# Optimization experiments

Measured on AMD Instinct MI355X. Metric: run time of the kernel, lower is better.

Reference implementation:

```python
import jax, jax.numpy as jnp
import numpy as np

E = 8        # num_experts
D_IN = 512   # num_inputs
H = 256      # num_neurons_expert
T = 64       # num_neurons_tower
B = 16384    # batch


def setup_inputs() -> dict:
    key = jax.random.key(0)
    ks = jax.random.split(key, 7)
    s_in = 1.0 / np.sqrt(D_IN)
    s_h = 1.0 / np.sqrt(H)
    return {
        "xv": jax.random.normal(ks[0], (B, D_IN), dtype=jnp.float32),
        # expert weights stacked: torch Linear weight is (out,in) -> (E, H, D_IN)
        "We": jax.random.uniform(ks[1], (E, H, D_IN), jnp.float32, -s_in, s_in),
        "be": jax.random.uniform(ks[2], (E, H), jnp.float32, -s_in, s_in),
        "Wg": jax.random.uniform(ks[3], (E, D_IN), jnp.float32, -s_in, s_in),
        "bg": jax.random.uniform(ks[4], (E,), jnp.float32, -s_in, s_in),
        "Wt": jax.random.uniform(ks[5], (T, H), jnp.float32, -s_h, s_h),
        "bt": jax.random.uniform(ks[6], (T,), jnp.float32, -s_h, s_h),
    }


def reference(xv, We, be, Wg, bg, Wt, bt):
    # All experts as one batched GEMM: [B,D] x [E,H,D] -> [B,E,H]
    experts = jax.nn.relu(jnp.einsum("bd,ehd->beh", xv, We) + be[None, :, :])
    # Dropout is identity in eval mode.
    gate = jax.nn.softmax(xv @ Wg.T + bg, axis=1)            # [B,E]
    combined = jnp.einsum("beh,be->bh", experts, gate)        # [B,H]
    out = jax.nn.sigmoid(combined @ Wt.T + bt)                # [B,T]
    return out
```

## Files before the change

### kernel.cpp

```cpp
#include <hip/hip_runtime.h>
#include <hip/hip_bf16.h>
#include <stdint.h>

typedef unsigned short u16;
typedef __bf16 bf16x8 __attribute__((ext_vector_type(8)));
typedef float f32x4 __attribute__((ext_vector_type(4)));

#define LDS_A_USH 8192
#define LDS_B_USH 16384

__device__ __forceinline__ void glds16(const void* g, void* l) {
  __builtin_amdgcn_global_load_lds(
      (const __attribute__((address_space(1))) unsigned int*)g,
      (__attribute__((address_space(3))) unsigned int*)l, 16, 0, 0);
}

__device__ __forceinline__ u16 f2bf(float f) {
  unsigned int u = __builtin_bit_cast(unsigned int, f);
  u += 0x7fffu + ((u >> 16) & 1u);
  return (u16)(u >> 16);
}

__global__ __launch_bounds__(256) void prep_kernel(
    const float* __restrict__ xv, const float* __restrict__ We,
    const float* __restrict__ Wg, const float* __restrict__ bg,
    const float* __restrict__ Wt,
    u16* __restrict__ xv_bf, u16* __restrict__ We_bf,
    u16* __restrict__ Wt_bf, float* __restrict__ gate) {
  const int bx = blockIdx.x;
  if (bx < 4096) {
    const int wid = threadIdx.x >> 6, lane = threadIdx.x & 63;
    const int row = bx * 4 + wid;
    const float* xr = xv + (row << 9) + lane * 8;
    float4 x0 = *(const float4*)xr;
    float4 x1 = *(const float4*)(xr + 4);
    uint4 o;
    o.x = (unsigned)f2bf(x0.x) | ((unsigned)f2bf(x0.y) << 16);
    o.y = (unsigned)f2bf(x0.z) | ((unsigned)f2bf(x0.w) << 16);
    o.z = (unsigned)f2bf(x1.x) | ((unsigned)f2bf(x1.y) << 16);
    o.w = (unsigned)f2bf(x1.z) | ((unsigned)f2bf(x1.w) << 16);
    *(uint4*)(xv_bf + (row << 9) + lane * 8) = o;
    float s[8];
#pragma unroll
    for (int e = 0; e < 8; e++) {
      const float* wg = Wg + (e << 9) + lane * 8;
      float4 w0 = *(const float4*)wg;
      float4 w1 = *(const float4*)(wg + 4);
      s[e] = x0.x * w0.x + x0.y * w0.y + x0.z * w0.z + x0.w * w0.w +
             x1.x * w1.x + x1.y * w1.y + x1.z * w1.z + x1.w * w1.w;
    }
#pragma unroll
    for (int e = 0; e < 8; e++) {
#pragma unroll
      for (int off = 32; off > 0; off >>= 1) s[e] += __shfl_xor(s[e], off);
      s[e] += bg[e];
    }
    float mx = s[0];
#pragma unroll
    for (int e = 1; e < 8; e++) mx = fmaxf(mx, s[e]);
    float p[8], sum = 0.f;
#pragma unroll
    for (int e = 0; e < 8; e++) { p[e] = __expf(s[e] - mx); sum += p[e]; }
    float inv = 1.f / sum;
    if (lane == 0) {
      float4 g0 = {p[0] * inv, p[1] * inv, p[2] * inv, p[3] * inv};
      float4 g1 = {p[4] * inv, p[5] * inv, p[6] * inv, p[7] * inv};
      *(float4*)(gate + row * 8) = g0;
      *(float4*)(gate + row * 8 + 4) = g1;
    }
  } else {
    const int base = (bx - 4096) * 2048 + threadIdx.x * 8;
    const float* src;
    u16* dst;
    if (base < 1048576) { src = We + base; dst = We_bf + base; }
    else { src = Wt + (base - 1048576); dst = Wt_bf + (base - 1048576); }
    float4 a = *(const float4*)src;
    float4 b = *(const float4*)(src + 4);
    uint4 o;
    o.x = (unsigned)f2bf(a.x) | ((unsigned)f2bf(a.y) << 16);
    o.y = (unsigned)f2bf(a.z) | ((unsigned)f2bf(a.w) << 16);
    o.z = (unsigned)f2bf(b.x) | ((unsigned)f2bf(b.y) << 16);
    o.w = (unsigned)f2bf(b.z) | ((unsigned)f2bf(b.w) << 16);
    *(uint4*)dst = o;
  }
}

__global__ __launch_bounds__(256, 2) void moe_main(
    const u16* __restrict__ xv_bf, const u16* __restrict__ We_bf,
    const float* __restrict__ be, const float* __restrict__ gate,
    const u16* __restrict__ Wt_bf, float* __restrict__ part) {
  __shared__ u16 lds[LDS_A_USH + LDS_B_USH];

  const int bx = blockIdx.x;
  const int mb = bx >> 1;
  const int hb = bx & 1;
  const int m0 = mb << 6;
  const int tid = threadIdx.x;
  const int lane = tid & 63;
  const int wid = tid >> 6;
  const int wm = wid >> 1;
  const int wn = wid & 1;
  const int l15 = lane & 15;
  const int l4 = lane >> 4;

  f32x4 comb[2][4];
#pragma unroll
  for (int mt = 0; mt < 2; mt++)
#pragma unroll
    for (int nt = 0; nt < 4; nt++) comb[mt][nt] = {0.f, 0.f, 0.f, 0.f};

  for (int e = 0; e < 8; e++) {
    f32x4 acc[2][4];
#pragma unroll
    for (int mt = 0; mt < 2; mt++)
#pragma unroll
      for (int nt = 0; nt < 4; nt++) acc[mt][nt] = {0.f, 0.f, 0.f, 0.f};

    const u16* Wb = We_bf + (e << 17);
    for (int kc = 0; kc < 4; kc++) {
      __syncthreads();
      const int kofs = kc << 7;
#pragma unroll
      for (int r = 0; r < 4; r++) {
        int gi = r * 256 + tid;
        int m = gi >> 4, s = gi & 15;
        int g = (s & 8) | ((s & 7) ^ (m & 7));
        glds16(xv_bf + ((m0 + m) << 9) + kofs + (g << 3), &lds[gi << 3]);
      }
#pragma unroll
      for (int r = 0; r < 8; r++) {
        int gi = r * 256 + tid;
        int n = gi >> 4, s = gi & 15;
        int g = (s & 8) | ((s & 7) ^ (n & 7));
        glds16(Wb + (((hb << 7) + n) << 9) + kofs + (g << 3),
               &lds[LDS_A_USH + (gi << 3)]);
      }
      __syncthreads();
#pragma unroll
      for (int ks = 0; ks < 4; ks++) {
        const int gg = ks * 4 + l4;
        bf16x8 af[2], bfr[4];
#pragma unroll
        for (int mt = 0; mt < 2; mt++) {
          int row = wm * 32 + mt * 16 + l15;
          int slot = (gg & 8) | ((gg & 7) ^ (row & 7));
          af[mt] = *(const bf16x8*)&lds[(row << 7) + (slot << 3)];
        }
#pragma unroll
        for (int nt = 0; nt < 4; nt++) {
          int n = wn * 64 + nt * 16 + l15;
          int slot = (gg & 8) | ((gg & 7) ^ (n & 7));
          bfr[nt] = *(const bf16x8*)&lds[LDS_A_USH + (n << 7) + (slot << 3)];
        }
#pragma unroll
        for (int mt = 0; mt < 2; mt++)
#pragma unroll
          for (int nt = 0; nt < 4; nt++)
            acc[mt][nt] = __builtin_amdgcn_mfma_f32_16x16x32_bf16(
                af[mt], bfr[nt], acc[mt][nt], 0, 0, 0);
      }
    }
    float bev[4];
#pragma unroll
    for (int nt = 0; nt < 4; nt++)
      bev[nt] = be[(e << 8) + (hb << 7) + wn * 64 + nt * 16 + l15];
#pragma unroll
    for (int mt = 0; mt < 2; mt++) {
#pragma unroll
      for (int i = 0; i < 4; i++) {
        float g = gate[((m0 + wm * 32 + mt * 16 + l4 * 4 + i) << 3) + e];
#pragma unroll
        for (int nt = 0; nt < 4; nt++)
          comb[mt][nt][i] += g * fmaxf(acc[mt][nt][i] + bev[nt], 0.f);
      }
    }
  }

  __syncthreads();
#pragma unroll
  for (int mt = 0; mt < 2; mt++)
#pragma unroll
    for (int i = 0; i < 4; i++) {
      int row = wm * 32 + mt * 16 + l4 * 4 + i;
#pragma unroll
      for (int nt = 0; nt < 4; nt++) {
        int col = wn * 64 + nt * 16 + l15;
        __bf16 v = (__bf16)comb[mt][nt][i];
        lds[row * 136 + col] = __builtin_bit_cast(u16, v);
      }
    }
  __syncthreads();
  f32x4 tacc[4];
#pragma unroll
  for (int nt = 0; nt < 4; nt++) tacc[nt] = {0.f, 0.f, 0.f, 0.f};
  const u16* WtB = Wt_bf + (hb << 7);
#pragma unroll
  for (int kc = 0; kc < 4; kc++) {
    int ko = kc * 32 + l4 * 8;
    bf16x8 aT = *(const bf16x8*)&lds[(wid * 16 + l15) * 136 + ko];
#pragma unroll
    for (int nt = 0; nt < 4; nt++) {
      bf16x8 bT = *(const bf16x8*)&WtB[(nt * 16 + l15) * 256 + ko];
      tacc[nt] = __builtin_amdgcn_mfma_f32_16x16x32_bf16(aT, bT, tacc[nt], 0, 0, 0);
    }
  }
  float* pout = part + hb * 1048576;
#pragma unroll
  for (int nt = 0; nt < 4; nt++)
#pragma unroll
    for (int i = 0; i < 4; i++) {
      int grow = m0 + wid * 16 + l4 * 4 + i;
      pout[grow * 64 + nt * 16 + l15] = tacc[nt][i];
    }
}

__global__ __launch_bounds__(256) void finish_kernel(
    const float* __restrict__ part, const float* __restrict__ bt,
    float* __restrict__ out) {
  const int idx = (blockIdx.x * 256 + threadIdx.x) << 2;
  float4 a = *(const float4*)(part + idx);
  float4 b = *(const float4*)(part + 1048576 + idx);
  float4 c = *(const float4*)(bt + (idx & 63));
  float4 r;
  r.x = 1.f / (1.f + __expf(-(a.x + b.x + c.x)));
  r.y = 1.f / (1.f + __expf(-(a.y + b.y + c.y)));
  r.z = 1.f / (1.f + __expf(-(a.z + b.z + c.z)));
  r.w = 1.f / (1.f + __expf(-(a.w + b.w + c.w)));
  *(float4*)(out + idx) = r;
}

extern "C" void kernel_launch(void* const* d_in, const int* in_sizes, int n_in,
                              void* d_out, int out_size, void* d_ws, size_t ws_size,
                              hipStream_t stream) {
  const float* xv = (const float*)d_in[0];
  const float* We = (const float*)d_in[1];
  const float* be = (const float*)d_in[2];
  const float* Wg = (const float*)d_in[3];
  const float* bg = (const float*)d_in[4];
  const float* Wt = (const float*)d_in[5];
  const float* bt = (const float*)d_in[6];

  char* ws = (char*)d_ws;
  u16* xv_bf = (u16*)ws;
  u16* We_bf = (u16*)(ws + 16777216);
  u16* Wt_bf = (u16*)(ws + 18874368);
  float* gate = (float*)(ws + 18907136);
  float* part = (float*)(ws + 19431424);

  prep_kernel<<<4616, 256, 0, stream>>>(xv, We, Wg, bg, Wt, xv_bf, We_bf, Wt_bf, gate);
  moe_main<<<512, 256, 0, stream>>>(xv_bf, We_bf, be, gate, Wt_bf, part);
  finish_kernel<<<1024, 256, 0, stream>>>(part, bt, (float*)d_out);
}
```

Measured before the change: 152.4 us.

## Restructure MoE kernel: 128-row tiles, expert-group split, bf16 partials, separate gate kernel

The main kernel now uses 512-thread blocks on 128-row tiles. Each block covers one half of H and one group of 4 experts, holding per-expert accumulators so an A tile loaded into LDS is reused across 4 experts per K chunk. The gate softmax moves into its own kernel that reads the bf16 copy of xv. Partials are written as bf16 across 4 splits and summed in the finish kernel, which reduces partial-store traffic but adds bf16 rounding, an extra launch, and more register pressure from 32 accumulator tiles.

```diff
diff --git a/kernel.cpp b/kernel.cpp
--- a/kernel.cpp
+++ b/kernel.cpp
@@ -1,13 +1,13 @@
 #include <hip/hip_runtime.h>
-#include <hip/hip_bf16.h>
 #include <stdint.h>
 
 typedef unsigned short u16;
 typedef __bf16 bf16x8 __attribute__((ext_vector_type(8)));
 typedef float f32x4 __attribute__((ext_vector_type(4)));
 
-#define LDS_A_USH 8192
-#define LDS_B_USH 16384
+#define XV_N 8388608
+#define WE_N 1048576
+#define WT_N 16384
 
 __device__ __forceinline__ void glds16(const void* g, void* l) {
   __builtin_amdgcn_global_load_lds(
@@ -21,212 +21,262 @@
   return (u16)(u >> 16);
 }
 
-__global__ __launch_bounds__(256) void prep_kernel(
+__device__ __forceinline__ float bf2f(u16 u) {
+  return __builtin_bit_cast(float, ((unsigned int)u) << 16);
+}
+
+__global__ __launch_bounds__(256) void convert_kernel(
     const float* __restrict__ xv, const float* __restrict__ We,
-    const float* __restrict__ Wg, const float* __restrict__ bg,
-    const float* __restrict__ Wt,
-    u16* __restrict__ xv_bf, u16* __restrict__ We_bf,
-    u16* __restrict__ Wt_bf, float* __restrict__ gate) {
-  const int bx = blockIdx.x;
-  if (bx < 4096) {
-    const int wid = threadIdx.x >> 6, lane = threadIdx.x & 63;
-    const int row = bx * 4 + wid;
-    const float* xr = xv + (row << 9) + lane * 8;
-    float4 x0 = *(const float4*)xr;
-    float4 x1 = *(const float4*)(xr + 4);
-    uint4 o;
-    o.x = (unsigned)f2bf(x0.x) | ((unsigned)f2bf(x0.y) << 16);
-    o.y = (unsigned)f2bf(x0.z) | ((unsigned)f2bf(x0.w) << 16);
-    o.z = (unsigned)f2bf(x1.x) | ((unsigned)f2bf(x1.y) << 16);
-    o.w = (unsigned)f2bf(x1.z) | ((unsigned)f2bf(x1.w) << 16);
-    *(uint4*)(xv_bf + (row << 9) + lane * 8) = o;
-    float s[8];
+    const float* __restrict__ Wt, u16* __restrict__ dst) {
+  int idx = (blockIdx.x * 256 + threadIdx.x) * 8;
+  const float* src;
+  if (idx < XV_N) src = xv + idx;
+  else if (idx < XV_N + WE_N) src = We + (idx - XV_N);
+  else src = Wt + (idx - XV_N - WE_N);
+  float4 a = *(const float4*)src;
+  float4 b = *(const float4*)(src + 4);
+  uint4 o;
+  o.x = (unsigned)f2bf(a.x) | ((unsigned)f2bf(a.y) << 16);
+  o.y = (unsigned)f2bf(a.z) | ((unsigned)f2bf(a.w) << 16);
+  o.z = (unsigned)f2bf(b.x) | ((unsigned)f2bf(b.y) << 16);
+  o.w = (unsigned)f2bf(b.z) | ((unsigned)f2bf(b.w) << 16);
+  *(uint4*)(dst + idx) = o;
+}
+
+__global__ __launch_bounds__(256) void gate_kernel(
+    const u16* __restrict__ xv_bf, const float* __restrict__ Wg,
+    const float* __restrict__ bg, float* __restrict__ gate) {
+  const int tid = threadIdx.x, wid = tid >> 6, lane = tid & 63;
+  const int rsub = lane >> 3, ksub = lane & 7;
+  const int row = blockIdx.x * 32 + wid * 8 + rsub;
+  const u16* xr = xv_bf + row * 512 + ksub * 64;
+  float s[8] = {0.f, 0.f, 0.f, 0.f, 0.f, 0.f, 0.f, 0.f};
+#pragma unroll
+  for (int j = 0; j < 8; j++) {
+    uint4 xp = *(const uint4*)(xr + j * 8);
+    float x[8];
+    x[0] = bf2f((u16)xp.x); x[1] = bf2f((u16)(xp.x >> 16));
+    x[2] = bf2f((u16)xp.y); x[3] = bf2f((u16)(xp.y >> 16));
+    x[4] = bf2f((u16)xp.z); x[5] = bf2f((u16)(xp.z >> 16));
+    x[6] = bf2f((u16)xp.w); x[7] = bf2f((u16)(xp.w >> 16));
 #pragma unroll
     for (int e = 0; e < 8; e++) {
-      const float* wg = Wg + (e << 9) + lane * 8;
+      const float* wg = Wg + e * 512 + ksub * 64 + j * 8;
       float4 w0 = *(const float4*)wg;
       float4 w1 = *(const float4*)(wg + 4);
-      s[e] = x0.x * w0.x + x0.y * w0.y + x0.z * w0.z + x0.w * w0.w +
-             x1.x * w1.x + x1.y * w1.y + x1.z * w1.z + x1.w * w1.w;
-    }
-#pragma unroll
-    for (int e = 0; e < 8; e++) {
-#pragma unroll
-      for (int off = 32; off > 0; off >>= 1) s[e] += __shfl_xor(s[e], off);
-      s[e] += bg[e];
-    }
-    float mx = s[0];
-#pragma unroll
-    for (int e = 1; e < 8; e++) mx = fmaxf(mx, s[e]);
-    float p[8], sum = 0.f;
-#pragma unroll
-    for (int e = 0; e < 8; e++) { p[e] = __expf(s[e] - mx); sum += p[e]; }
-    float inv = 1.f / sum;
-    if (lane == 0) {
-      float4 g0 = {p[0] * inv, p[1] * inv, p[2] * inv, p[3] * inv};
-      float4 g1 = {p[4] * inv, p[5] * inv, p[6] * inv, p[7] * inv};
-      *(float4*)(gate + row * 8) = g0;
-      *(float4*)(gate + row * 8 + 4) = g1;
-    }
-  } else {
-    const int base = (bx - 4096) * 2048 + threadIdx.x * 8;
-    const float* src;
-    u16* dst;
-    if (base < 1048576) { src = We + base; dst = We_bf + base; }
-    else { src = Wt + (base - 1048576); dst = Wt_bf + (base - 1048576); }
-    float4 a = *(const float4*)src;
-    float4 b = *(const float4*)(src + 4);
-    uint4 o;
-    o.x = (unsigned)f2bf(a.x) | ((unsigned)f2bf(a.y) << 16);
-    o.y = (unsigned)f2bf(a.z) | ((unsigned)f2bf(a.w) << 16);
-    o.z = (unsigned)f2bf(b.x) | ((unsigned)f2bf(b.y) << 16);
-    o.w = (unsigned)f2bf(b.z) | ((unsigned)f2bf(b.w) << 16);
-    *(uint4*)dst = o;
-  }
-}
-
-__global__ __launch_bounds__(256, 2) void moe_main(
+      s[e] += x[0] * w0.x + x[1] * w0.y + x[2] * w0.z + x[3] * w0.w +
+              x[4] * w1.x + x[5] * w1.y + x[6] * w1.z + x[7] * w1.w;
+    }
+  }
+#pragma unroll
+  for (int e = 0; e < 8; e++) {
+    s[e] += __shfl_xor(s[e], 1);
+    s[e] += __shfl_xor(s[e], 2);
+    s[e] += __shfl_xor(s[e], 4);
+    s[e] += bg[e];
+  }
+  float mx = s[0];
+#pragma unroll
+  for (int e = 1; e < 8; e++) mx = fmaxf(mx, s[e]);
+  float p[8], sum = 0.f;
+#pragma unroll
+  for (int e = 0; e < 8; e++) { p[e] = __expf(s[e] - mx); sum += p[e]; }
+  float inv = 1.f / sum;
+  if (ksub == 0) {
+    float4 g0 = {p[0] * inv, p[1] * inv, p[2] * inv, p[3] * inv};
+    float4 g1 = {p[4] * inv, p[5] * inv, p[6] * inv, p[7] * inv};
+    *(float4*)(gate + row * 8) = g0;
+    *(float4*)(gate + row * 8 + 4) = g1;
+  }
+}
+
+__global__ __launch_bounds__(512, 2) void moe_main(
     const u16* __restrict__ xv_bf, const u16* __restrict__ We_bf,
     const float* __restrict__ be, const float* __restrict__ gate,
-    const u16* __restrict__ Wt_bf, float* __restrict__ part) {
-  __shared__ u16 lds[LDS_A_USH + LDS_B_USH];
+    const u16* __restrict__ Wt_bf, u16* __restrict__ part) {
+  __shared__ u16 lds[24576];
 
   const int bx = blockIdx.x;
-  const int mb = bx >> 1;
-  const int hb = bx & 1;
-  const int m0 = mb << 6;
-  const int tid = threadIdx.x;
-  const int lane = tid & 63;
-  const int wid = tid >> 6;
-  const int wm = wid >> 1;
-  const int wn = wid & 1;
-  const int l15 = lane & 15;
-  const int l4 = lane >> 4;
-
-  f32x4 comb[2][4];
-#pragma unroll
-  for (int mt = 0; mt < 2; mt++)
-#pragma unroll
-    for (int nt = 0; nt < 4; nt++) comb[mt][nt] = {0.f, 0.f, 0.f, 0.f};
-
-  for (int e = 0; e < 8; e++) {
-    f32x4 acc[2][4];
-#pragma unroll
-    for (int mt = 0; mt < 2; mt++)
-#pragma unroll
-      for (int nt = 0; nt < 4; nt++) acc[mt][nt] = {0.f, 0.f, 0.f, 0.f};
-
-    const u16* Wb = We_bf + (e << 17);
-    for (int kc = 0; kc < 4; kc++) {
-      __syncthreads();
-      const int kofs = kc << 7;
-#pragma unroll
-      for (int r = 0; r < 4; r++) {
-        int gi = r * 256 + tid;
-        int m = gi >> 4, s = gi & 15;
-        int g = (s & 8) | ((s & 7) ^ (m & 7));
-        glds16(xv_bf + ((m0 + m) << 9) + kofs + (g << 3), &lds[gi << 3]);
-      }
-#pragma unroll
-      for (int r = 0; r < 8; r++) {
-        int gi = r * 256 + tid;
-        int n = gi >> 4, s = gi & 15;
-        int g = (s & 8) | ((s & 7) ^ (n & 7));
-        glds16(Wb + (((hb << 7) + n) << 9) + kofs + (g << 3),
-               &lds[LDS_A_USH + (gi << 3)]);
-      }
-      __syncthreads();
-#pragma unroll
-      for (int ks = 0; ks < 4; ks++) {
-        const int gg = ks * 4 + l4;
-        bf16x8 af[2], bfr[4];
-#pragma unroll
-        for (int mt = 0; mt < 2; mt++) {
-          int row = wm * 32 + mt * 16 + l15;
-          int slot = (gg & 8) | ((gg & 7) ^ (row & 7));
-          af[mt] = *(const bf16x8*)&lds[(row << 7) + (slot << 3)];
+  const int mb = bx & 127, sub = bx >> 7;
+  const int ep = sub >> 1, hb = sub & 1;
+  const int m0 = mb << 7, h0 = hb << 7, eg0 = ep << 2;
+  const int tid = threadIdx.x, lane = tid & 63, wid = tid >> 6;
+  const int wm = wid >> 2, wn = wid & 3;
+  const int l15 = lane & 15, l4 = lane >> 4;
+
+  f32x4 acc[4][4][2];
+#pragma unroll
+  for (int e = 0; e < 4; e++)
+#pragma unroll
+    for (int mt = 0; mt < 4; mt++)
+#pragma unroll
+      for (int nt = 0; nt < 2; nt++) acc[e][mt][nt] = {0.f, 0.f, 0.f, 0.f};
+
+  for (int kc = 0; kc < 8; kc++) {
+    const int kofs = kc << 6;
+    __syncthreads();
+#pragma unroll
+    for (int r = 0; r < 2; r++) {
+      int gi = r * 512 + tid;
+      int row = gi >> 3, s = gi & 7, g = s ^ (row & 7);
+      glds16(xv_bf + ((m0 + row) << 9) + kofs + (g << 3), &lds[gi << 3]);
+    }
+#pragma unroll
+    for (int r = 0; r < 4; r++) {
+      int gi = r * 512 + tid;
+      int el = gi >> 10, rem = gi & 1023, n = rem >> 3, s = rem & 7, g = s ^ (n & 7);
+      glds16(We_bf + ((eg0 + el) << 17) + ((h0 + n) << 9) + kofs + (g << 3),
+             &lds[8192 + (gi << 3)]);
+    }
+    __syncthreads();
+    bf16x8 af[4][2];
+#pragma unroll
+    for (int mt = 0; mt < 4; mt++)
+#pragma unroll
+      for (int ks = 0; ks < 2; ks++) {
+        int row = wm * 64 + mt * 16 + l15;
+        int gg = ks * 4 + l4;
+        int slot = gg ^ (row & 7);
+        af[mt][ks] = *(const bf16x8*)&lds[(row << 6) + (slot << 3)];
+      }
+#pragma unroll
+    for (int el = 0; el < 2; el++)
+#pragma unroll
+      for (int ks = 0; ks < 2; ks++) {
+        bf16x8 bf[2];
+#pragma unroll
+        for (int nt = 0; nt < 2; nt++) {
+          int n = wn * 32 + nt * 16 + l15;
+          int gg = ks * 4 + l4;
+          int slot = gg ^ (n & 7);
+          bf[nt] = *(const bf16x8*)&lds[8192 + (el << 13) + (n << 6) + (slot << 3)];
         }
 #pragma unroll
-        for (int nt = 0; nt < 4; nt++) {
-          int n = wn * 64 + nt * 16 + l15;
-          int slot = (gg & 8) | ((gg & 7) ^ (n & 7));
-          bfr[nt] = *(const bf16x8*)&lds[LDS_A_USH + (n << 7) + (slot << 3)];
+        for (int mt = 0; mt < 4; mt++)
+#pragma unroll
+          for (int nt = 0; nt < 2; nt++)
+            acc[el][mt][nt] = __builtin_amdgcn_mfma_f32_16x16x32_bf16(
+                af[mt][ks], bf[nt], acc[el][mt][nt], 0, 0, 0);
+      }
+    __syncthreads();
+#pragma unroll
+    for (int r = 0; r < 4; r++) {
+      int gi = r * 512 + tid;
+      int el = gi >> 10, rem = gi & 1023, n = rem >> 3, s = rem & 7, g = s ^ (n & 7);
+      glds16(We_bf + ((eg0 + 2 + el) << 17) + ((h0 + n) << 9) + kofs + (g << 3),
+             &lds[8192 + (gi << 3)]);
+    }
+    __syncthreads();
+#pragma unroll
+    for (int el = 0; el < 2; el++)
+#pragma unroll
+      for (int ks = 0; ks < 2; ks++) {
+        bf16x8 bf[2];
+#pragma unroll
+        for (int nt = 0; nt < 2; nt++) {
+          int n = wn * 32 + nt * 16 + l15;
+          int gg = ks * 4 + l4;
+          int slot = gg ^ (n & 7);
+          bf[nt] = *(const bf16x8*)&lds[8192 + (el << 13) + (n << 6) + (slot << 3)];
         }
 #pragma unroll
-        for (int mt = 0; mt < 2; mt++)
-#pragma unroll
-          for (int nt = 0; nt < 4; nt++)
-            acc[mt][nt] = __builtin_amdgcn_mfma_f32_16x16x32_bf16(
-                af[mt], bfr[nt], acc[mt][nt], 0, 0, 0);
-      }
-    }
-    float bev[4];
-#pragma unroll
-    for (int nt = 0; nt < 4; nt++)
-      bev[nt] = be[(e << 8) + (hb << 7) + wn * 64 + nt * 16 + l15];
-#pragma unroll
-    for (int mt = 0; mt < 2; mt++) {
-#pragma unroll
-      for (int i = 0; i < 4; i++) {
-        float g = gate[((m0 + wm * 32 + mt * 16 + l4 * 4 + i) << 3) + e];
-#pragma unroll
-        for (int nt = 0; nt < 4; nt++)
-          comb[mt][nt][i] += g * fmaxf(acc[mt][nt][i] + bev[nt], 0.f);
+        for (int mt = 0; mt < 4; mt++)
+#pragma unroll
+          for (int nt = 0; nt < 2; nt++)
+            acc[2 + el][mt][nt] = __builtin_amdgcn_mfma_f32_16x16x32_bf16(
+                af[mt][ks], bf[nt], acc[2 + el][mt][nt], 0, 0, 0);
+      }
+  }
+
+  float bev[4][2];
+#pragma unroll
+  for (int e = 0; e < 4; e++)
+#pragma unroll
+    for (int nt = 0; nt < 2; nt++)
+      bev[e][nt] = be[(eg0 + e) * 256 + h0 + wn * 32 + nt * 16 + l15];
+
+  f32x4 comb[4][2];
+#pragma unroll
+  for (int mt = 0; mt < 4; mt++) {
+#pragma unroll
+    for (int i = 0; i < 4; i++) {
+      int row = m0 + wm * 64 + mt * 16 + l4 * 4 + i;
+      float4 gv4 = *(const float4*)&gate[(row << 3) + eg0];
+      const float* gv = &gv4.x;
+#pragma unroll
+      for (int nt = 0; nt < 2; nt++) {
+        float c = 0.f;
+#pragma unroll
+        for (int e = 0; e < 4; e++)
+          c += gv[e] * fmaxf(acc[e][mt][nt][i] + bev[e][nt], 0.f);
+        comb[mt][nt][i] = c;
       }
     }
   }
 
   __syncthreads();
 #pragma unroll
-  for (int mt = 0; mt < 2; mt++)
+  for (int mt = 0; mt < 4; mt++)
 #pragma unroll
     for (int i = 0; i < 4; i++) {
-      int row = wm * 32 + mt * 16 + l4 * 4 + i;
-#pragma unroll
-      for (int nt = 0; nt < 4; nt++) {
-        int col = wn * 64 + nt * 16 + l15;
-        __bf16 v = (__bf16)comb[mt][nt][i];
-        lds[row * 136 + col] = __builtin_bit_cast(u16, v);
+      int row = wm * 64 + mt * 16 + l4 * 4 + i;
+#pragma unroll
+      for (int nt = 0; nt < 2; nt++) {
+        int col = wn * 32 + nt * 16 + l15;
+        lds[row * 136 + col] = f2bf(comb[mt][nt][i]);
       }
     }
   __syncthreads();
   f32x4 tacc[4];
 #pragma unroll
   for (int nt = 0; nt < 4; nt++) tacc[nt] = {0.f, 0.f, 0.f, 0.f};
-  const u16* WtB = Wt_bf + (hb << 7);
-#pragma unroll
-  for (int kc = 0; kc < 4; kc++) {
-    int ko = kc * 32 + l4 * 8;
-    bf16x8 aT = *(const bf16x8*)&lds[(wid * 16 + l15) * 136 + ko];
+  const int trow = wid * 16 + l15;
+#pragma unroll
+  for (int ks = 0; ks < 4; ks++) {
+    bf16x8 aT = *(const bf16x8*)&lds[trow * 136 + ks * 32 + l4 * 8];
 #pragma unroll
     for (int nt = 0; nt < 4; nt++) {
-      bf16x8 bT = *(const bf16x8*)&WtB[(nt * 16 + l15) * 256 + ko];
+      bf16x8 bT = *(const bf16x8*)&Wt_bf[(nt * 16 + l15) * 256 + h0 + ks * 32 + l4 * 8];
       tacc[nt] = __builtin_amdgcn_mfma_f32_16x16x32_bf16(aT, bT, tacc[nt], 0, 0, 0);
     }
   }
-  float* pout = part + hb * 1048576;
+  u16* pout = part + sub * 1048576;
 #pragma unroll
   for (int nt = 0; nt < 4; nt++)
 #pragma unroll
     for (int i = 0; i < 4; i++) {
       int grow = m0 + wid * 16 + l4 * 4 + i;
-      pout[grow * 64 + nt * 16 + l15] = tacc[nt][i];
+      pout[grow * 64 + nt * 16 + l15] = f2bf(tacc[nt][i]);
     }
 }
 
 __global__ __launch_bounds__(256) void finish_kernel(
-    const float* __restrict__ part, const float* __restrict__ bt,
+    const u16* __restrict__ part, const float* __restrict__ bt,
     float* __restrict__ out) {
-  const int idx = (blockIdx.x * 256 + threadIdx.x) << 2;
-  float4 a = *(const float4*)(part + idx);
-  float4 b = *(const float4*)(part + 1048576 + idx);
-  float4 c = *(const float4*)(bt + (idx & 63));
-  float4 r;
-  r.x = 1.f / (1.f + __expf(-(a.x + b.x + c.x)));
-  r.y = 1.f / (1.f + __expf(-(a.y + b.y + c.y)));
-  r.z = 1.f / (1.f + __expf(-(a.z + b.z + c.z)));
-  r.w = 1.f / (1.f + __expf(-(a.w + b.w + c.w)));
-  *(float4*)(out + idx) = r;
+  const int base = (blockIdx.x * 256 + threadIdx.x) * 8;
+  float a[8] = {0.f, 0.f, 0.f, 0.f, 0.f, 0.f, 0.f, 0.f};
+#pragma unroll
+  for (int s = 0; s < 4; s++) {
+    uint4 p = *(const uint4*)(part + s * 1048576 + base);
+    a[0] += bf2f((u16)p.x); a[1] += bf2f((u16)(p.x >> 16));
+    a[2] += bf2f((u16)p.y); a[3] += bf2f((u16)(p.y >> 16));
+    a[4] += bf2f((u16)p.z); a[5] += bf2f((u16)(p.z >> 16));
+    a[6] += bf2f((u16)p.w); a[7] += bf2f((u16)(p.w >> 16));
+  }
+  const int t0 = base & 63;
+  float4 b0 = *(const float4*)(bt + t0);
+  float4 b1 = *(const float4*)(bt + t0 + 4);
+  const float* bb = &b0.x;
+  float r[8];
+#pragma unroll
+  for (int j = 0; j < 8; j++) {
+    float bj = (j < 4) ? bb[j] : (&b1.x)[j - 4];
+    r[j] = 1.f / (1.f + __expf(-(a[j] + bj)));
+  }
+  float4 o0 = {r[0], r[1], r[2], r[3]};
+  float4 o1 = {r[4], r[5], r[6], r[7]};
+  *(float4*)(out + base) = o0;
+  *(float4*)(out + base + 4) = o1;
 }
 
 extern "C" void kernel_launch(void* const* d_in, const int* in_sizes, int n_in,
@@ -241,13 +291,15 @@
   const float* bt = (const float*)d_in[6];
 
   char* ws = (char*)d_ws;
-  u16* xv_bf = (u16*)ws;
-  u16* We_bf = (u16*)(ws + 16777216);
-  u16* Wt_bf = (u16*)(ws + 18874368);
+  u16* cvt = (u16*)ws;
+  u16* xv_bf = cvt;
+  u16* We_bf = cvt + XV_N;
+  u16* Wt_bf = cvt + XV_N + WE_N;
   float* gate = (float*)(ws + 18907136);
-  float* part = (float*)(ws + 19431424);
-
-  prep_kernel<<<4616, 256, 0, stream>>>(xv, We, Wg, bg, Wt, xv_bf, We_bf, Wt_bf, gate);
-  moe_main<<<512, 256, 0, stream>>>(xv_bf, We_bf, be, gate, Wt_bf, part);
-  finish_kernel<<<1024, 256, 0, stream>>>(part, bt, (float*)d_out);
-}
+  u16* part = (u16*)(ws + 19431424);
+
+  convert_kernel<<<4616, 256, 0, stream>>>(xv, We, Wt, cvt);
+  gate_kernel<<<512, 256, 0, stream>>>(xv_bf, Wg, bg, gate);
+  moe_main<<<512, 512, 0, stream>>>(xv_bf, We_bf, be, gate, Wt_bf, part);
+  finish_kernel<<<512, 256, 0, stream>>>(part, bt, (float*)d_out);
+}
```

New measurement: 178.5 us. +17.1%, slower.
